# Kernel optimization log

Hardware: AMD Instinct MI355X
Metric: run time of the kernel (lower is better)

Reference implementation:

```python
import jax, jax.numpy as jnp
import numpy as np

S, B, H, NL = 2048, 32, 1024, 2


def setup_inputs() -> dict:
    key = jax.random.key(0)
    k1, k2, k3, k4, k5 = jax.random.split(key, 5)
    hidden = jax.random.normal(k1, (NL, B, H), dtype=jnp.float32)
    encoder_outputs = jax.random.normal(k2, (S, B, H), dtype=jnp.float32)
    # nn.Linear(2H, H): weight [H, 2H], bias [H]
    attn_w = jax.random.normal(k3, (H, 2 * H), dtype=jnp.float32) / np.sqrt(2.0 * H)
    attn_b = jax.random.normal(k4, (H,), dtype=jnp.float32) * 0.01
    # v ~ N(0, 1/sqrt(H))
    v = jax.random.normal(k5, (H,), dtype=jnp.float32) / np.sqrt(H)
    return {"hidden": hidden, "encoder_outputs": encoder_outputs,
            "attn_w": attn_w, "attn_b": attn_b, "v": v}


def reference(hidden, encoder_outputs, attn_w, attn_b, v):
    # hidden: [NL, B, H]; encoder_outputs: [S, B, H]
    max_len = encoder_outputs.shape[0]
    h = jnp.broadcast_to(hidden[-1], (max_len,) + hidden[-1].shape)  # [S, B, H]
    x = jnp.concatenate([h, encoder_outputs], axis=2)                 # [S, B, 2H]
    energy = jnp.tanh(jnp.einsum('sbk,hk->sbh', x, attn_w) + attn_b)  # [S, B, H]
    scores = jnp.einsum('sbh,h->bs', energy, v)                       # [B, S]
    return jax.nn.softmax(scores, axis=1)
```

## Files before the change

kernel.cpp:

```cpp
#include <hip/hip_runtime.h>
#include <stdint.h>


#define S_LEN 2048
#define B_SZ 32
#define H_SZ 1024
#define M_TOT (S_LEN * B_SZ)
#define K_TOT H_SZ
#define NCB 8
#define BK 64
#define TILE_SHORTS 8192

typedef __attribute__((ext_vector_type(8))) short short8;
typedef __attribute__((ext_vector_type(4))) float f32x4;

static __device__ __forceinline__ unsigned short f2bf(float x) {
  uint32_t u = __builtin_bit_cast(uint32_t, x);
  u += 0x7FFFu + ((u >> 16) & 1u);
  return (unsigned short)(u >> 16);
}
static __device__ __forceinline__ uint32_t pack2(float a, float b) {
  return (uint32_t)f2bf(a) | ((uint32_t)f2bf(b) << 16);
}
static __device__ __forceinline__ float fast_tanh(float x) {
  float e = __expf(2.0f * x);
  return 1.0f - 2.0f / (e + 1.0f);
}

__global__ void __launch_bounds__(256) prep_u_kernel(
    const float* __restrict__ hidden, const float* __restrict__ attn_w,
    const float* __restrict__ attn_b, float* __restrict__ u) {
  __shared__ float hs[H_SZ];
  const int b = blockIdx.y, hc = blockIdx.x, tid = threadIdx.x;
  const float* hid = hidden + (size_t)1 * B_SZ * H_SZ + (size_t)b * H_SZ;
  for (int i = tid; i < H_SZ; i += 256) hs[i] = hid[i];
  __syncthreads();
  const int h = hc * 256 + tid;
  const float* wrow = attn_w + (size_t)h * (2 * H_SZ);
  float s = 0.f;
#pragma unroll 4
  for (int k = 0; k < H_SZ; k += 4) {
    float4 w4 = *reinterpret_cast<const float4*>(wrow + k);
    s += w4.x * hs[k] + w4.y * hs[k + 1] + w4.z * hs[k + 2] + w4.w * hs[k + 3];
  }
  u[(size_t)b * H_SZ + h] = s + attn_b[h];
}

__global__ void __launch_bounds__(256) prep_a_kernel(
    const float* __restrict__ enc, unsigned short* __restrict__ Aimg) {
  const int idx = blockIdx.x * 256 + threadIdx.x;
  const int m = idx >> 7, sl = idx & 127;
  const int kb = sl >> 3, s8 = sl & 7;
  const float4* src =
      reinterpret_cast<const float4*>(enc + (size_t)m * K_TOT + kb * BK + s8 * 8);
  float4 f0 = src[0], f1 = src[1];
  uint4 o;
  o.x = pack2(f0.x, f0.y); o.y = pack2(f0.z, f0.w);
  o.z = pack2(f1.x, f1.y); o.w = pack2(f1.z, f1.w);
  const int row = m & 127;
  const size_t tile = (size_t)(m >> 7) * 16 + kb;
  unsigned short* dst = Aimg + tile * TILE_SHORTS + row * 64 + ((s8 ^ (row & 7)) << 3);
  *reinterpret_cast<uint4*>(dst) = o;
}

__global__ void __launch_bounds__(256) prep_b_kernel(
    const float* __restrict__ attn_w, unsigned short* __restrict__ Bimg) {
  const int idx = blockIdx.x * 256 + threadIdx.x;
  const int n = idx >> 7, sl = idx & 127;
  const int kb = sl >> 3, s8 = sl & 7;
  const float4* src = reinterpret_cast<const float4*>(
      attn_w + (size_t)n * 2048 + 1024 + kb * BK + s8 * 8);
  float4 f0 = src[0], f1 = src[1];
  uint4 o;
  o.x = pack2(f0.x, f0.y); o.y = pack2(f0.z, f0.w);
  o.z = pack2(f1.x, f1.y); o.w = pack2(f1.z, f1.w);
  const int row = n & 127;
  const size_t tile = (size_t)(n >> 7) * 16 + kb;
  unsigned short* dst = Bimg + tile * TILE_SHORTS + row * 64 + ((s8 ^ (row & 7)) << 3);
  *reinterpret_cast<uint4*>(dst) = o;
}

__global__ void __launch_bounds__(256) gemm_img_kernel(
    const unsigned short* __restrict__ Aimg, const unsigned short* __restrict__ Bimg,
    const float* __restrict__ u, const float* __restrict__ v,
    float* __restrict__ pscore) {
  __shared__ unsigned short As[TILE_SHORTS];
  __shared__ unsigned short Bs[TILE_SHORTS];
  __shared__ float rowsum[2][128];

  const int tid = threadIdx.x;
  const int wid = tid >> 6, lane = tid & 63;
  const int wr = wid >> 1, wc = wid & 1;

  const int wg = blockIdx.x;
  const int xcd = wg & 7, li = wg >> 3;
  const int rp = xcd * 64 + (li >> 3);
  const int cb = li & 7;
  const int brow = rp * 128, bcol = cb * 128;

  const unsigned short* Ag = Aimg + (size_t)rp * 16 * TILE_SHORTS;
  const unsigned short* Bg = Bimg + (size_t)cb * 16 * TILE_SHORTS;

  f32x4 acc[4][4];
#pragma unroll
  for (int i = 0; i < 4; ++i)
#pragma unroll
    for (int j = 0; j < 4; ++j) acc[i][j] = (f32x4){0.f, 0.f, 0.f, 0.f};

  const int fr = lane & 15, g = lane >> 4;
  const int soff0 = ((g) ^ (fr & 7)) << 3;
  const int soff1 = ((4 + g) ^ (fr & 7)) << 3;
  const int arow_base = (wr * 64 + fr) * 64;
  const int brow_base = (wc * 64 + fr) * 64;
  const int stg = wid * 2048;

  for (int kb = 0; kb < 16; ++kb) {
    __syncthreads();
    const unsigned short* at = Ag + kb * TILE_SHORTS + stg + lane * 8;
    const unsigned short* bt = Bg + kb * TILE_SHORTS + stg + lane * 8;
#pragma unroll
    for (int j = 0; j < 4; ++j) {
      __builtin_amdgcn_global_load_lds(
          (const __attribute__((address_space(1))) void*)(at + j * 512),
          (__attribute__((address_space(3))) void*)(As + stg + j * 512), 16, 0, 0);
      __builtin_amdgcn_global_load_lds(
          (const __attribute__((address_space(1))) void*)(bt + j * 512),
          (__attribute__((address_space(3))) void*)(Bs + stg + j * 512), 16, 0, 0);
    }
    __syncthreads();

    short8 af[4], bf[4];
#pragma unroll
    for (int i = 0; i < 4; ++i)
      af[i] = *reinterpret_cast<const short8*>(As + arow_base + i * 1024 + soff0);
#pragma unroll
    for (int j = 0; j < 4; ++j)
      bf[j] = *reinterpret_cast<const short8*>(Bs + brow_base + j * 1024 + soff0);
#pragma unroll
    for (int i = 0; i < 4; ++i)
#pragma unroll
      for (int j = 0; j < 4; ++j)
        acc[i][j] = __builtin_amdgcn_mfma_f32_16x16x32_bf16(af[i], bf[j], acc[i][j], 0, 0, 0);
#pragma unroll
    for (int i = 0; i < 4; ++i)
      af[i] = *reinterpret_cast<const short8*>(As + arow_base + i * 1024 + soff1);
#pragma unroll
    for (int j = 0; j < 4; ++j)
      bf[j] = *reinterpret_cast<const short8*>(Bs + brow_base + j * 1024 + soff1);
#pragma unroll
    for (int i = 0; i < 4; ++i)
#pragma unroll
      for (int j = 0; j < 4; ++j)
        acc[i][j] = __builtin_amdgcn_mfma_f32_16x16x32_bf16(af[i], bf[j], acc[i][j], 0, 0, 0);
  }

  float vv[4];
#pragma unroll
  for (int j = 0; j < 4; ++j) vv[j] = v[bcol + wc * 64 + j * 16 + fr];

  const int g4 = g * 4;
#pragma unroll
  for (int i = 0; i < 4; ++i) {
#pragma unroll
    for (int reg = 0; reg < 4; ++reg) {
      const int rloc = wr * 64 + i * 16 + g4 + reg;
      const int bb = (brow + rloc) & (B_SZ - 1);
      float rs = 0.f;
#pragma unroll
      for (int j = 0; j < 4; ++j) {
        const int h = bcol + wc * 64 + j * 16 + fr;
        float val = acc[i][j][reg] + u[(size_t)bb * H_SZ + h];
        rs += vv[j] * fast_tanh(val);
      }
      rs += __shfl_xor(rs, 1);
      rs += __shfl_xor(rs, 2);
      rs += __shfl_xor(rs, 4);
      rs += __shfl_xor(rs, 8);
      if (fr == 0) rowsum[wc][rloc] = rs;
    }
  }
  __syncthreads();
  if (tid < 128)
    pscore[(size_t)cb * M_TOT + brow + tid] = rowsum[0][tid] + rowsum[1][tid];
}

__global__ void __launch_bounds__(256) prep_w2_flat_kernel(
    const float* __restrict__ attn_w, unsigned short* __restrict__ Bt) {
  const int idx = blockIdx.x * 256 + threadIdx.x;
  const int base = idx * 4;
  const int n = base >> 10, k = base & 1023;
  float4 w = *reinterpret_cast<const float4*>(attn_w + (size_t)n * 2048 + 1024 + k);
  ushort4 o;
  o.x = f2bf(w.x); o.y = f2bf(w.y); o.z = f2bf(w.z); o.w = f2bf(w.w);
  *reinterpret_cast<ushort4*>(Bt + base) = o;
}

__global__ void __launch_bounds__(256) gemm_fused_kernel(
    const float* __restrict__ A, const unsigned short* __restrict__ Bt,
    const float* __restrict__ u, const float* __restrict__ v,
    float* __restrict__ pscore) {
  __shared__ unsigned short As[128 * 32];
  __shared__ unsigned short Bs[128 * 32];
  __shared__ float rowsum[2][128];
  const int tid = threadIdx.x;
  const int wid = tid >> 6, lane = tid & 63;
  const int wr = wid >> 1, wc = wid & 1;
  const int cb = blockIdx.x;
  const int brow = blockIdx.y * 128;
  const int bcol = cb * 128;
  const int arow_st = tid >> 1;
  const int acol_st = (tid & 1) * 16;
  const float* Ag = A + (size_t)(brow + arow_st) * K_TOT + acol_st;
  unsigned short* AsW = As + arow_st * 32 + acol_st;
  const int chunk0 = wid * 2;
  const unsigned short* Bg0 =
      Bt + (size_t)(bcol + chunk0 * 16 + (lane >> 2)) * K_TOT + (lane & 3) * 8;
  f32x4 acc[4][4];
#pragma unroll
  for (int i = 0; i < 4; ++i)
#pragma unroll
    for (int j = 0; j < 4; ++j) acc[i][j] = (f32x4){0.f, 0.f, 0.f, 0.f};
  const int fr = lane & 15;
  const int kseg = (lane >> 4) * 8;
  for (int k0 = 0; k0 < K_TOT; k0 += 32) {
    __syncthreads();
    const float4* ap = reinterpret_cast<const float4*>(Ag + k0);
    float4 f0 = ap[0], f1 = ap[1], f2 = ap[2], f3 = ap[3];
    uint4 w0, w1;
    w0.x = pack2(f0.x, f0.y); w0.y = pack2(f0.z, f0.w);
    w0.z = pack2(f1.x, f1.y); w0.w = pack2(f1.z, f1.w);
    w1.x = pack2(f2.x, f2.y); w1.y = pack2(f2.z, f2.w);
    w1.z = pack2(f3.x, f3.y); w1.w = pack2(f3.z, f3.w);
    *reinterpret_cast<uint4*>(AsW) = w0;
    *reinterpret_cast<uint4*>(AsW + 8) = w1;
    __builtin_amdgcn_global_load_lds(
        (const __attribute__((address_space(1))) void*)(Bg0 + k0),
        (__attribute__((address_space(3))) void*)(Bs + chunk0 * 512), 16, 0, 0);
    __builtin_amdgcn_global_load_lds(
        (const __attribute__((address_space(1))) void*)(Bg0 + 16 * K_TOT + k0),
        (__attribute__((address_space(3))) void*)(Bs + chunk0 * 512 + 512), 16, 0, 0);
    __syncthreads();
    short8 af[4], bf[4];
#pragma unroll
    for (int i = 0; i < 4; ++i)
      af[i] = *reinterpret_cast<const short8*>(As + (wr * 64 + i * 16 + fr) * 32 + kseg);
#pragma unroll
    for (int j = 0; j < 4; ++j)
      bf[j] = *reinterpret_cast<const short8*>(Bs + (wc * 64 + j * 16 + fr) * 32 + kseg);
#pragma unroll
    for (int i = 0; i < 4; ++i)
#pragma unroll
      for (int j = 0; j < 4; ++j)
        acc[i][j] = __builtin_amdgcn_mfma_f32_16x16x32_bf16(af[i], bf[j], acc[i][j], 0, 0, 0);
  }
  float vv[4];
#pragma unroll
  for (int j = 0; j < 4; ++j) vv[j] = v[bcol + wc * 64 + j * 16 + fr];
  const int g4 = (lane >> 4) * 4;
#pragma unroll
  for (int i = 0; i < 4; ++i) {
#pragma unroll
    for (int reg = 0; reg < 4; ++reg) {
      const int rloc = wr * 64 + i * 16 + g4 + reg;
      const int bb = (brow + rloc) & (B_SZ - 1);
      float rs = 0.f;
#pragma unroll
      for (int j = 0; j < 4; ++j) {
        const int h = bcol + wc * 64 + j * 16 + fr;
        float val = acc[i][j][reg] + u[(size_t)bb * H_SZ + h];
        rs += vv[j] * fast_tanh(val);
      }
      rs += __shfl_xor(rs, 1);
      rs += __shfl_xor(rs, 2);
      rs += __shfl_xor(rs, 4);
      rs += __shfl_xor(rs, 8);
      if (fr == 0) rowsum[wc][rloc] = rs;
    }
  }
  __syncthreads();
  if (tid < 128)
    pscore[(size_t)cb * M_TOT + brow + tid] = rowsum[0][tid] + rowsum[1][tid];
}

__global__ void __launch_bounds__(256) softmax_kernel(
    const float* __restrict__ ps, float* __restrict__ out) {
  const int b = blockIdx.x, tid = threadIdx.x;
  const int wid = tid >> 6, lane = tid & 63;
  __shared__ float sred[4];
  float vals[8];
  float mx = -1e30f;
#pragma unroll
  for (int ii = 0; ii < 8; ++ii) {
    const int s = ii * 256 + tid;
    float sum = 0.f;
#pragma unroll
    for (int cbk = 0; cbk < NCB; ++cbk) sum += ps[(size_t)cbk * M_TOT + s * B_SZ + b];
    vals[ii] = sum;
    mx = fmaxf(mx, sum);
  }
#pragma unroll
  for (int m = 1; m < 64; m <<= 1) mx = fmaxf(mx, __shfl_xor(mx, m));
  if (lane == 0) sred[wid] = mx;
  __syncthreads();
  mx = fmaxf(fmaxf(sred[0], sred[1]), fmaxf(sred[2], sred[3]));
  __syncthreads();
  float es = 0.f;
#pragma unroll
  for (int ii = 0; ii < 8; ++ii) {
    vals[ii] = __expf(vals[ii] - mx);
    es += vals[ii];
  }
#pragma unroll
  for (int m = 1; m < 64; m <<= 1) es += __shfl_xor(es, m);
  if (lane == 0) sred[wid] = es;
  __syncthreads();
  es = sred[0] + sred[1] + sred[2] + sred[3];
  const float inv = 1.0f / es;
#pragma unroll
  for (int ii = 0; ii < 8; ++ii) out[(size_t)b * S_LEN + ii * 256 + tid] = vals[ii] * inv;
}

extern "C" void kernel_launch(void* const* d_in, const int* in_sizes, int n_in,
                              void* d_out, int out_size, void* d_ws, size_t ws_size,
                              hipStream_t stream) {
  const float* hidden = (const float*)d_in[0];
  const float* enc    = (const float*)d_in[1];
  const float* attn_w = (const float*)d_in[2];
  const float* attn_b = (const float*)d_in[3];
  const float* v      = (const float*)d_in[4];
  float* out = (float*)d_out;

  const size_t A_BYTES = (size_t)M_TOT * K_TOT * 2;
  const size_t B_BYTES = (size_t)K_TOT * K_TOT * 2;
  const size_t U_BYTES = (size_t)B_SZ * H_SZ * 4;
  const size_t P_BYTES = (size_t)NCB * M_TOT * 4;
  char* w = (char*)d_ws;

  if (ws_size >= A_BYTES + B_BYTES + U_BYTES + P_BYTES) {
    unsigned short* Aimg = (unsigned short*)w;
    unsigned short* Bimg = (unsigned short*)(w + A_BYTES);
    float* u  = (float*)(w + A_BYTES + B_BYTES);
    float* ps = (float*)(w + A_BYTES + B_BYTES + U_BYTES);
    prep_u_kernel<<<dim3(4, 32), 256, 0, stream>>>(hidden, attn_w, attn_b, u);
    prep_b_kernel<<<512, 256, 0, stream>>>(attn_w, Bimg);
    prep_a_kernel<<<M_TOT * 128 / 256, 256, 0, stream>>>(enc, Aimg);
    gemm_img_kernel<<<NCB * (M_TOT / 128), 256, 0, stream>>>(Aimg, Bimg, u, v, ps);
    softmax_kernel<<<B_SZ, 256, 0, stream>>>(ps, out);
  } else {
    unsigned short* Bt = (unsigned short*)w;
    float* u  = (float*)(w + B_BYTES);
    float* ps = (float*)(w + B_BYTES + U_BYTES);
    prep_u_kernel<<<dim3(4, 32), 256, 0, stream>>>(hidden, attn_w, attn_b, u);
    prep_w2_flat_kernel<<<1024, 256, 0, stream>>>(attn_w, Bt);
    gemm_fused_kernel<<<dim3(NCB, M_TOT / 128), 256, 0, stream>>>(enc, Bt, u, v, ps);
    softmax_kernel<<<B_SZ, 256, 0, stream>>>(ps, out);
  }
}
```

Measured before the change: 350.4 us.

## Double-buffer LDS tiles in GEMM and batch four rows per prep_u block

The GEMM main loop now uses two LDS buffers per operand. The next K tile's global-to-LDS load is issued before computing on the current tile, so memory latency overlaps with MFMA work, and the launch bounds request two blocks per CU. Separately, prep_u now handles four batch rows per block, reusing each loaded weight float4 across four dot products and cutting redundant reads of attn_w. The cost is double the LDS footprint, roughly 66KB per block, which may limit occupancy, plus explicit waitcnt and barrier handling that must stay correct.

```diff
diff --git a/kernel.cpp b/kernel.cpp
--- a/kernel.cpp
+++ b/kernel.cpp
@@ -30,20 +30,31 @@
 __global__ void __launch_bounds__(256) prep_u_kernel(
     const float* __restrict__ hidden, const float* __restrict__ attn_w,
     const float* __restrict__ attn_b, float* __restrict__ u) {
-  __shared__ float hs[H_SZ];
-  const int b = blockIdx.y, hc = blockIdx.x, tid = threadIdx.x;
-  const float* hid = hidden + (size_t)1 * B_SZ * H_SZ + (size_t)b * H_SZ;
-  for (int i = tid; i < H_SZ; i += 256) hs[i] = hid[i];
+  __shared__ float hs[4][H_SZ];
+  const int hc = blockIdx.x;
+  const int bg = blockIdx.y;
+  const int tid = threadIdx.x;
+  for (int i = tid; i < 4 * H_SZ; i += 256) {
+    const int bi = i >> 10, k = i & 1023;
+    hs[bi][k] = hidden[(size_t)B_SZ * H_SZ + (size_t)(bg * 4 + bi) * H_SZ + k];
+  }
   __syncthreads();
   const int h = hc * 256 + tid;
   const float* wrow = attn_w + (size_t)h * (2 * H_SZ);
-  float s = 0.f;
+  float s0 = 0.f, s1 = 0.f, s2 = 0.f, s3 = 0.f;
 #pragma unroll 4
   for (int k = 0; k < H_SZ; k += 4) {
     float4 w4 = *reinterpret_cast<const float4*>(wrow + k);
-    s += w4.x * hs[k] + w4.y * hs[k + 1] + w4.z * hs[k + 2] + w4.w * hs[k + 3];
-  }
-  u[(size_t)b * H_SZ + h] = s + attn_b[h];
+    s0 += w4.x * hs[0][k] + w4.y * hs[0][k + 1] + w4.z * hs[0][k + 2] + w4.w * hs[0][k + 3];
+    s1 += w4.x * hs[1][k] + w4.y * hs[1][k + 1] + w4.z * hs[1][k + 2] + w4.w * hs[1][k + 3];
+    s2 += w4.x * hs[2][k] + w4.y * hs[2][k + 1] + w4.z * hs[2][k + 2] + w4.w * hs[2][k + 3];
+    s3 += w4.x * hs[3][k] + w4.y * hs[3][k + 1] + w4.z * hs[3][k + 2] + w4.w * hs[3][k + 3];
+  }
+  const float bb = attn_b[h];
+  u[(size_t)(bg * 4 + 0) * H_SZ + h] = s0 + bb;
+  u[(size_t)(bg * 4 + 1) * H_SZ + h] = s1 + bb;
+  u[(size_t)(bg * 4 + 2) * H_SZ + h] = s2 + bb;
+  u[(size_t)(bg * 4 + 3) * H_SZ + h] = s3 + bb;
 }
 
 __global__ void __launch_bounds__(256) prep_a_kernel(
@@ -80,12 +91,16 @@
   *reinterpret_cast<uint4*>(dst) = o;
 }
 
-__global__ void __launch_bounds__(256) gemm_img_kernel(
+#define LGKM0 asm volatile("s_waitcnt lgkmcnt(0)" ::: "memory")
+#define VM0   asm volatile("s_waitcnt vmcnt(0)" ::: "memory")
+#define BARRIER __builtin_amdgcn_s_barrier()
+
+__global__ void __launch_bounds__(256, 2) gemm_img_kernel(
     const unsigned short* __restrict__ Aimg, const unsigned short* __restrict__ Bimg,
     const float* __restrict__ u, const float* __restrict__ v,
     float* __restrict__ pscore) {
-  __shared__ unsigned short As[TILE_SHORTS];
-  __shared__ unsigned short Bs[TILE_SHORTS];
+  __shared__ unsigned short As[2][TILE_SHORTS];
+  __shared__ unsigned short Bs[2][TILE_SHORTS];
   __shared__ float rowsum[2][128];
 
   const int tid = threadIdx.x;
@@ -114,45 +129,73 @@
   const int brow_base = (wc * 64 + fr) * 64;
   const int stg = wid * 2048;
 
-  for (int kb = 0; kb < 16; ++kb) {
-    __syncthreads();
-    const unsigned short* at = Ag + kb * TILE_SHORTS + stg + lane * 8;
-    const unsigned short* bt = Bg + kb * TILE_SHORTS + stg + lane * 8;
-#pragma unroll
-    for (int j = 0; j < 4; ++j) {
-      __builtin_amdgcn_global_load_lds(
-          (const __attribute__((address_space(1))) void*)(at + j * 512),
-          (__attribute__((address_space(3))) void*)(As + stg + j * 512), 16, 0, 0);
-      __builtin_amdgcn_global_load_lds(
-          (const __attribute__((address_space(1))) void*)(bt + j * 512),
-          (__attribute__((address_space(3))) void*)(Bs + stg + j * 512), 16, 0, 0);
-    }
-    __syncthreads();
-
-    short8 af[4], bf[4];
-#pragma unroll
-    for (int i = 0; i < 4; ++i)
-      af[i] = *reinterpret_cast<const short8*>(As + arow_base + i * 1024 + soff0);
-#pragma unroll
-    for (int j = 0; j < 4; ++j)
-      bf[j] = *reinterpret_cast<const short8*>(Bs + brow_base + j * 1024 + soff0);
-#pragma unroll
-    for (int i = 0; i < 4; ++i)
-#pragma unroll
-      for (int j = 0; j < 4; ++j)
-        acc[i][j] = __builtin_amdgcn_mfma_f32_16x16x32_bf16(af[i], bf[j], acc[i][j], 0, 0, 0);
-#pragma unroll
-    for (int i = 0; i < 4; ++i)
-      af[i] = *reinterpret_cast<const short8*>(As + arow_base + i * 1024 + soff1);
-#pragma unroll
-    for (int j = 0; j < 4; ++j)
-      bf[j] = *reinterpret_cast<const short8*>(Bs + brow_base + j * 1024 + soff1);
-#pragma unroll
-    for (int i = 0; i < 4; ++i)
-#pragma unroll
-      for (int j = 0; j < 4; ++j)
-        acc[i][j] = __builtin_amdgcn_mfma_f32_16x16x32_bf16(af[i], bf[j], acc[i][j], 0, 0, 0);
-  }
+#define STAGE(BUF, KB)                                                          \
+  do {                                                                          \
+    const unsigned short* at_ = Ag + (KB) * TILE_SHORTS + stg + lane * 8;       \
+    const unsigned short* bt_ = Bg + (KB) * TILE_SHORTS + stg + lane * 8;       \
+    _Pragma("unroll")                                                           \
+    for (int j_ = 0; j_ < 4; ++j_) {                                            \
+      __builtin_amdgcn_global_load_lds(                                         \
+          (const __attribute__((address_space(1))) void*)(at_ + j_ * 512),      \
+          (__attribute__((address_space(3))) void*)(&As[BUF][stg + j_ * 512]),  \
+          16, 0, 0);                                                            \
+      __builtin_amdgcn_global_load_lds(                                         \
+          (const __attribute__((address_space(1))) void*)(bt_ + j_ * 512),      \
+          (__attribute__((address_space(3))) void*)(&Bs[BUF][stg + j_ * 512]),  \
+          16, 0, 0);                                                            \
+    }                                                                           \
+  } while (0)
+
+#define COMPUTE(BUF)                                                            \
+  do {                                                                          \
+    short8 af[4], bf[4];                                                        \
+    _Pragma("unroll")                                                           \
+    for (int i_ = 0; i_ < 4; ++i_)                                              \
+      af[i_] = *reinterpret_cast<const short8*>(                                \
+          &As[BUF][arow_base + i_ * 1024 + soff0]);                             \
+    _Pragma("unroll")                                                           \
+    for (int j_ = 0; j_ < 4; ++j_)                                              \
+      bf[j_] = *reinterpret_cast<const short8*>(                                \
+          &Bs[BUF][brow_base + j_ * 1024 + soff0]);                             \
+    _Pragma("unroll")                                                           \
+    for (int i_ = 0; i_ < 4; ++i_)                                              \
+      _Pragma("unroll")                                                         \
+      for (int j_ = 0; j_ < 4; ++j_)                                            \
+        acc[i_][j_] = __builtin_amdgcn_mfma_f32_16x16x32_bf16(                  \
+            af[i_], bf[j_], acc[i_][j_], 0, 0, 0);                              \
+    _Pragma("unroll")                                                           \
+    for (int i_ = 0; i_ < 4; ++i_)                                              \
+      af[i_] = *reinterpret_cast<const short8*>(                                \
+          &As[BUF][arow_base + i_ * 1024 + soff1]);                             \
+    _Pragma("unroll")                                                           \
+    for (int j_ = 0; j_ < 4; ++j_)                                              \
+      bf[j_] = *reinterpret_cast<const short8*>(                                \
+          &Bs[BUF][brow_base + j_ * 1024 + soff1]);                             \
+    _Pragma("unroll")                                                           \
+    for (int i_ = 0; i_ < 4; ++i_)                                              \
+      _Pragma("unroll")                                                         \
+      for (int j_ = 0; j_ < 4; ++j_)                                            \
+        acc[i_][j_] = __builtin_amdgcn_mfma_f32_16x16x32_bf16(                  \
+            af[i_], bf[j_], acc[i_][j_], 0, 0, 0);                              \
+  } while (0)
+
+  STAGE(0, 0);
+  VM0;
+  BARRIER;
+  for (int kb = 0; kb < 16; kb += 2) {
+    STAGE(1, kb + 1);
+    COMPUTE(0);
+    LGKM0;
+    VM0;
+    BARRIER;
+    if (kb + 2 < 16) STAGE(0, kb + 2);
+    COMPUTE(1);
+    LGKM0;
+    VM0;
+    BARRIER;
+  }
+#undef STAGE
+#undef COMPUTE
 
   float vv[4];
 #pragma unroll
@@ -341,7 +384,7 @@
     unsigned short* Bimg = (unsigned short*)(w + A_BYTES);
     float* u  = (float*)(w + A_BYTES + B_BYTES);
     float* ps = (float*)(w + A_BYTES + B_BYTES + U_BYTES);
-    prep_u_kernel<<<dim3(4, 32), 256, 0, stream>>>(hidden, attn_w, attn_b, u);
+    prep_u_kernel<<<dim3(4, 8), 256, 0, stream>>>(hidden, attn_w, attn_b, u);
     prep_b_kernel<<<512, 256, 0, stream>>>(attn_w, Bimg);
     prep_a_kernel<<<M_TOT * 128 / 256, 256, 0, stream>>>(enc, Aimg);
     gemm_img_kernel<<<NCB * (M_TOT / 128), 256, 0, stream>>>(Aimg, Bimg, u, v, ps);
@@ -350,7 +393,7 @@
     unsigned short* Bt = (unsigned short*)w;
     float* u  = (float*)(w + B_BYTES);
     float* ps = (float*)(w + B_BYTES + U_BYTES);
-    prep_u_kernel<<<dim3(4, 32), 256, 0, stream>>>(hidden, attn_w, attn_b, u);
+    prep_u_kernel<<<dim3(4, 8), 256, 0, stream>>>(hidden, attn_w, attn_b, u);
     prep_w2_flat_kernel<<<1024, 256, 0, stream>>>(attn_w, Bt);
     gemm_fused_kernel<<<dim3(NCB, M_TOT / 128), 256, 0, stream>>>(enc, Bt, u, v, ps);
     softmax_kernel<<<B_SZ, 256, 0, stream>>>(ps, out);
```

Result: slower. 375.3 us (+7.1%).
